# Performance work log

Hardware: AMD Instinct MI355X
Metric: run time of the kernel (lower is better)

The kernel has to match this reference:

```python
import jax, jax.numpy as jnp
import numpy as np

B, S, D, H = 2, 2048, 512, 8
DK = D // H  # 64


def setup_inputs() -> dict:
    key = jax.random.key(0)
    ks = jax.random.split(key, 16)
    def t(k):
        return jax.random.normal(k, (B, S, D), dtype=jnp.float32)
    inp = {
        'query_real': t(ks[0]), 'key_real': t(ks[1]), 'value_real': t(ks[2]),
        'query_phase': t(ks[3]), 'key_phase': t(ks[4]), 'value_phase': t(ks[5]),
        'mask': jax.random.randint(ks[6], (B, 1, S), 0, 2, dtype=jnp.int32),
    }
    # Four distinct linear layers (clones deepcopies); real and phase paths share them.
    for i, nm in enumerate(['q', 'k', 'v', 'o']):
        inp['W' + nm] = jax.random.normal(ks[7 + 2 * i], (D, D), dtype=jnp.float32) * 0.02
        inp['b' + nm] = jax.random.normal(ks[8 + 2 * i], (D,), dtype=jnp.float32) * 0.02
    return inp


def _lin(x, W, b):
    # nn.Linear: x @ W.T + b
    return jnp.einsum('bsd,ed->bse', x, W) + b


def _heads(x):
    # [B,S,D] -> [B,H,S,DK]
    return jnp.swapaxes(x.reshape(B, S, H, DK), 1, 2)


def reference(query_real, key_real, value_real, query_phase, key_phase, value_phase,
              mask, Wq, bq, Wk, bk, Wv, bv, Wo, bo):
    qr = _heads(_lin(query_real, Wq, bq)); qp = _heads(_lin(query_phase, Wq, bq))
    kr = _heads(_lin(key_real, Wk, bk));   kp = _heads(_lin(key_phase, Wk, bk))
    vr = _heads(_lin(value_real, Wv, bv)); vp = _heads(_lin(value_phase, Wv, bv))

    # complex QK^T: 4 matmuls -> real/imag parts, magnitude score
    sr = jnp.einsum('bhqd,bhkd->bhqk', qr, kr) - jnp.einsum('bhqd,bhkd->bhqk', qp, kp)
    sp = jnp.einsum('bhqd,bhkd->bhqk', qr, kp) + jnp.einsum('bhqd,bhkd->bhqk', qp, kr)
    scores = jnp.sqrt(sr * sr + sp * sp) / jnp.sqrt(jnp.float32(DK))
    # mask [B,1,S] -> unsqueeze head dim -> [B,1,1,S]
    scores = jnp.where(mask[:, None] == 0, jnp.float32(-1e9), scores)
    p = jax.nn.softmax(scores, axis=-1)

    xr = jnp.einsum('bhqk,bhkd->bhqd', p, vr)
    xp = jnp.einsum('bhqk,bhkd->bhqd', p, vp)
    xr = jnp.swapaxes(xr, 1, 2).reshape(B, S, D)
    xp = jnp.swapaxes(xp, 1, 2).reshape(B, S, D)
    return _lin(xr, Wo, bo), _lin(xp, Wo, bo)
```

## Files before the change

kernel.cpp:

```cpp
#include <hip/hip_runtime.h>

typedef __bf16 bf16;
typedef __bf16 bf16x8 __attribute__((ext_vector_type(8)));
typedef float  f32x4  __attribute__((ext_vector_type(4)));

static constexpr int CB = 2;
static constexpr int CS = 2048;
static constexpr int CD = 512;
static constexpr int CH = 8;
static constexpr int CDK = 64;
static constexpr int NROWS = CB * CH * CS;
static constexpr size_t NT = (size_t)CB * CS * CD;
static constexpr size_t WN = (size_t)CD * CD;

__device__ __forceinline__ f32x4 mfma16(bf16x8 a, bf16x8 b, f32x4 c) {
    return __builtin_amdgcn_mfma_f32_16x16x32_bf16(a, b, c, 0, 0, 0);
}

__device__ __forceinline__ bf16x8 cvt8(const float* __restrict__ p) {
    float4 x0 = *reinterpret_cast<const float4*>(p);
    float4 x1 = *reinterpret_cast<const float4*>(p + 4);
    bf16x8 r;
    r[0] = (bf16)x0.x; r[1] = (bf16)x0.y; r[2] = (bf16)x0.z; r[3] = (bf16)x0.w;
    r[4] = (bf16)x1.x; r[5] = (bf16)x1.y; r[6] = (bf16)x1.z; r[7] = (bf16)x1.w;
    return r;
}

__device__ __forceinline__ void gload16(const void* g, void* l) {
    __builtin_amdgcn_global_load_lds(
        (const __attribute__((address_space(1))) void*)g,
        (__attribute__((address_space(3))) void*)l, 16, 0, 0);
}

struct CvtP {
    const float* src[10];
    bf16* dst[10];
    int n8[10];
};
__global__ __launch_bounds__(256) void cvt_kernel(CvtP C) {
    const int t = blockIdx.y;
    const int i = blockIdx.x * 256 + threadIdx.x;
    if (i < C.n8[t])
        *reinterpret_cast<bf16x8*>(C.dst[t] + (size_t)i * 8) =
            cvt8(C.src[t] + (size_t)i * 8);
}

struct PB {
    const bf16* A[6];
    const bf16* W[6];
    const float* bias[6];
    bf16* dst[6];
    int mode[6];
};
__global__ __launch_bounds__(256) void projb_kernel(PB P) {
    __shared__ uint4 tile[2][2][512];

    const int z = blockIdx.z;
    const bf16* __restrict__ A = P.A[z];
    const bf16* __restrict__ W = P.W[z];
    const float* __restrict__ bias = P.bias[z];
    bf16* __restrict__ dst = P.dst[z];
    const int mode = P.mode[z];

    const int m0 = blockIdx.x * 64, n0 = blockIdx.y * 64;
    const int tid = threadIdx.x;
    const int lane = tid & 63, w = tid >> 6;
    const int wm = w >> 1, wn = w & 1;
    const int l16 = lane & 15, lhi = lane >> 4;

    const int tensor = w >> 1, half = w & 1;
    const int rlo = lane >> 3, slotL = lane & 7;
    const bf16* gbase = tensor ? W : A;
    const int t0 = tensor ? n0 : m0;
    const char* gp = (const char*)gbase
                   + (size_t)(t0 + half*32 + rlo) * (CD * 2)
                   + (size_t)((slotL ^ rlo) * 16);

    auto stage = [&](int buf, int kk) {
        const char* p = gp + (size_t)kk * 128;
        uint4* ld = &tile[buf][tensor][half * 256];
        #pragma unroll
        for (int i = 0; i < 4; ++i)
            gload16(p + (size_t)i * 8 * (CD * 2), ld + i * 64);
    };

    f32x4 acc[2][2] = {};

    stage(0, 0);
    asm volatile("s_waitcnt vmcnt(0)" ::: "memory");
    __syncthreads();

    for (int kk = 0; kk < 8; ++kk) {
        if (kk + 1 < 8) stage((kk + 1) & 1, kk + 1);

        const uint4* aT = &tile[kk & 1][0][0];
        const uint4* bT = &tile[kk & 1][1][0];
        #pragma unroll
        for (int ks = 0; ks < 2; ++ks) {
            const int c = ks*4 + lhi;
            const int ra0 = wm*32 + l16, ra1 = ra0 + 16;
            const int rb0 = wn*32 + l16, rb1 = rb0 + 16;
            bf16x8 af0 = __builtin_bit_cast(bf16x8, aT[ra0*8 + (c ^ (ra0 & 7))]);
            bf16x8 af1 = __builtin_bit_cast(bf16x8, aT[ra1*8 + (c ^ (ra1 & 7))]);
            bf16x8 bg0 = __builtin_bit_cast(bf16x8, bT[rb0*8 + (c ^ (rb0 & 7))]);
            bf16x8 bg1 = __builtin_bit_cast(bf16x8, bT[rb1*8 + (c ^ (rb1 & 7))]);
            acc[0][0] = mfma16(af0, bg0, acc[0][0]);
            acc[0][1] = mfma16(af0, bg1, acc[0][1]);
            acc[1][0] = mfma16(af1, bg0, acc[1][0]);
            acc[1][1] = mfma16(af1, bg1, acc[1][1]);
        }
        if (kk + 1 < 8) __syncthreads();
    }

    #pragma unroll
    for (int ms = 0; ms < 2; ++ms)
    #pragma unroll
    for (int ns = 0; ns < 2; ++ns) {
        const int col = n0 + wn*32 + ns*16 + l16;
        const float bv = bias[col];
        const int hh = col >> 6, dk = col & 63;
        #pragma unroll
        for (int i = 0; i < 4; ++i) {
            const int m = m0 + wm*32 + ms*16 + lhi*4 + i;
            const float v = acc[ms][ns][i] + bv;
            const int b = m >> 11, s = m & 2047;
            if (mode == 0)
                dst[(((size_t)(b*CH + hh)) * CS + s) * CDK + dk] = (bf16)v;
            else
                dst[(((size_t)(b*CH + hh)) * CDK + dk) * CS + s] = (bf16)v;
        }
    }
}

__global__ __launch_bounds__(256) void oprojb_kernel(
    const bf16* __restrict__ Xr, const bf16* __restrict__ Xp,
    const bf16* __restrict__ Wo, const float* __restrict__ bo,
    float* __restrict__ out)
{
    __shared__ uint4 tile[2][2][512];

    const bf16* __restrict__ A = blockIdx.z ? Xp : Xr;
    float* __restrict__ dst = out + (size_t)blockIdx.z * NT;

    const int m0 = blockIdx.x * 64, n0 = blockIdx.y * 64;
    const int tid = threadIdx.x;
    const int lane = tid & 63, w = tid >> 6;
    const int wm = w >> 1, wn = w & 1;
    const int l16 = lane & 15, lhi = lane >> 4;

    const int tensor = w >> 1, half = w & 1;
    const int rlo = lane >> 3, slotL = lane & 7;
    const bf16* gbase = tensor ? Wo : A;
    const int t0 = tensor ? n0 : m0;
    const char* gp = (const char*)gbase
                   + (size_t)(t0 + half*32 + rlo) * (CD * 2)
                   + (size_t)((slotL ^ rlo) * 16);

    auto stage = [&](int buf, int kk) {
        const char* p = gp + (size_t)kk * 128;
        uint4* ld = &tile[buf][tensor][half * 256];
        #pragma unroll
        for (int i = 0; i < 4; ++i)
            gload16(p + (size_t)i * 8 * (CD * 2), ld + i * 64);
    };

    f32x4 acc[2][2] = {};

    stage(0, 0);
    asm volatile("s_waitcnt vmcnt(0)" ::: "memory");
    __syncthreads();

    for (int kk = 0; kk < 8; ++kk) {
        if (kk + 1 < 8) stage((kk + 1) & 1, kk + 1);

        const uint4* aT = &tile[kk & 1][0][0];
        const uint4* bT = &tile[kk & 1][1][0];
        #pragma unroll
        for (int ks = 0; ks < 2; ++ks) {
            const int c = ks*4 + lhi;
            const int ra0 = wm*32 + l16, ra1 = ra0 + 16;
            const int rb0 = wn*32 + l16, rb1 = rb0 + 16;
            bf16x8 af0 = __builtin_bit_cast(bf16x8, aT[ra0*8 + (c ^ (ra0 & 7))]);
            bf16x8 af1 = __builtin_bit_cast(bf16x8, aT[ra1*8 + (c ^ (ra1 & 7))]);
            bf16x8 bg0 = __builtin_bit_cast(bf16x8, bT[rb0*8 + (c ^ (rb0 & 7))]);
            bf16x8 bg1 = __builtin_bit_cast(bf16x8, bT[rb1*8 + (c ^ (rb1 & 7))]);
            acc[0][0] = mfma16(af0, bg0, acc[0][0]);
            acc[0][1] = mfma16(af0, bg1, acc[0][1]);
            acc[1][0] = mfma16(af1, bg0, acc[1][0]);
            acc[1][1] = mfma16(af1, bg1, acc[1][1]);
        }
        if (kk + 1 < 8) __syncthreads();
    }

    #pragma unroll
    for (int ms = 0; ms < 2; ++ms)
    #pragma unroll
    for (int ns = 0; ns < 2; ++ns) {
        const int col = n0 + wn*32 + ns*16 + l16;
        const float bv = bo[col];
        #pragma unroll
        for (int i = 0; i < 4; ++i) {
            const int m = m0 + wm*32 + ms*16 + lhi*4 + i;
            dst[(size_t)m * 512 + col] = acc[ms][ns][i] + bv;
        }
    }
}

__global__ __launch_bounds__(512, 4) void attn_kernel(
    const bf16* __restrict__ Qr, const bf16* __restrict__ Qp,
    const bf16* __restrict__ Kr, const bf16* __restrict__ Kp,
    const bf16* __restrict__ Vtr, const bf16* __restrict__ Vtp,
    const int* __restrict__ mask, int lognsp,
    float* __restrict__ POR, float* __restrict__ POP, float* __restrict__ PLs)
{
    __shared__ uint4 stg[2][4][512];

    const int F = blockIdx.x;
    const int qt = (F >> 3) & 15;
    const int g  = (F & 7) | ((F >> 7) << 3);
    const int bh = g >> lognsp, z = g & ((1 << lognsp) - 1);
    const int Lkv = CS >> lognsp, kvbase = z * Lkv;
    const int nt = Lkv >> 6;
    const int b = bh >> 3;
    const size_t base = (size_t)bh * CS * CDK;

    const int tid = threadIdx.x, lane = tid & 63, w = tid >> 6;
    const int l16 = lane & 15, lhi = lane >> 4;
    const int q0 = qt * 128 + w * 16;

    const int tensor = w >> 1, half = w & 1;
    const int rlo = lane >> 3, slotL = lane & 7;
    const int chunkL = slotL ^ rlo;
    const char* gsrc = (tensor == 0) ? (const char*)Kr : (tensor == 1) ? (const char*)Kp
                     : (tensor == 2) ? (const char*)Vtr : (const char*)Vtp;
    size_t laneoff, iStride, tStride;
    if (tensor < 2) {
        laneoff = base*2 + (size_t)(kvbase + half*32 + rlo) * 128 + chunkL*16;
        iStride = 8 * 128;  tStride = 8192;
    } else {
        laneoff = base*2 + (size_t)(half*32 + rlo) * (CS*2) + (size_t)kvbase*2 + chunkL*16;
        iStride = 8 * CS * 2;  tStride = 128;
    }
    const char* gp = gsrc + laneoff;

    auto stage = [&](int bi, int t) {
        const char* p = gp + (size_t)t * tStride;
        uint4* ldst = &stg[bi][tensor][half * 256];
        #pragma unroll
        for (int i = 0; i < 4; ++i)
            gload16(p + i*iStride, ldst + i*64);
    };

    stage(0, 0);

    bf16x8 qrf[2], qpf[2], qnf[2];
    #pragma unroll
    for (int ks = 0; ks < 2; ++ks) {
        const size_t qoff = base + (size_t)(q0 + l16) * CDK + ks*32 + lhi*8;
        qrf[ks] = *reinterpret_cast<const bf16x8*>(&Qr[qoff]);
        qpf[ks] = *reinterpret_cast<const bf16x8*>(&Qp[qoff]);
        uint4 t = __builtin_bit_cast(uint4, qpf[ks]);
        t.x ^= 0x80008000u; t.y ^= 0x80008000u; t.z ^= 0x80008000u; t.w ^= 0x80008000u;
        qnf[ks] = __builtin_bit_cast(bf16x8, t);
    }

    unsigned long long keepA[8] = {};
    for (int t = 0; t < nt; ++t) {
        const unsigned long long m64 =
            __ballot(mask[b*CS + kvbase + t*64 + lane] != 0);
        const unsigned long long s = m64 >> (lhi * 4);
        const unsigned int k16 = (unsigned int)(s & 0xFull)
                               | ((unsigned int)((s >> 16) & 0xFull) << 4)
                               | ((unsigned int)((s >> 32) & 0xFull) << 8)
                               | ((unsigned int)((s >> 48) & 0xFull) << 12);
        keepA[t >> 2] |= (unsigned long long)k16 << ((t & 3) * 16);
    }

    f32x4 oR[4] = {}, oP[4] = {};
    float lpart = 0.f;

    asm volatile("s_waitcnt vmcnt(0)" ::: "memory");
    __syncthreads();

    for (int t = 0; t < nt; ++t) {
        if (t + 1 < nt) stage((t + 1) & 1, t + 1);

        const int bi = t & 1;
        const unsigned int k16 = (unsigned int)(keepA[t >> 2] >> ((t & 3) * 16)) & 0xFFFFu;
        const uint4* kTr = &stg[bi][0][0];
        const uint4* kTp = &stg[bi][1][0];
        const uint4* vTr = &stg[bi][2][0];
        const uint4* vTp = &stg[bi][3][0];

        float pp[4][4];
        #pragma unroll
        for (int kb = 0; kb < 4; ++kb) {
            const int krow = kb*16 + l16;
            f32x4 aR = {}, aP = {};
            __builtin_amdgcn_s_setprio(1);
            #pragma unroll
            for (int ks = 0; ks < 2; ++ks) {
                const int ci = krow*8 + ((ks*4 + lhi) ^ (krow & 7));
                const bf16x8 kr8 = __builtin_bit_cast(bf16x8, kTr[ci]);
                const bf16x8 kp8 = __builtin_bit_cast(bf16x8, kTp[ci]);
                aR = mfma16(kr8, qrf[ks], aR);
                aR = mfma16(kp8, qnf[ks], aR);
                aP = mfma16(kr8, qpf[ks], aP);
                aP = mfma16(kp8, qrf[ks], aP);
            }
            __builtin_amdgcn_s_setprio(0);
            #pragma unroll
            for (int i = 0; i < 4; ++i) {
                const float sr = aR[i], sp = aP[i];
                const float mag = __builtin_amdgcn_sqrtf(fmaf(sr, sr, sp*sp));
                float p = __builtin_amdgcn_exp2f(fmaf(mag, 0.18033688f, -5.77078016f));
                p = ((k16 >> (kb*4 + i)) & 1u) ? p : 0.0f;
                pp[kb][i] = p;
                lpart += p;
            }
        }

        #pragma unroll
        for (int c = 0; c < 2; ++c) {
            unsigned int r0, r1, r2, r3;
            asm("v_cvt_pk_bf16_f32 %0, %1, %2" : "=v"(r0) : "v"(pp[2*c][0]),   "v"(pp[2*c][1]));
            asm("v_cvt_pk_bf16_f32 %0, %1, %2" : "=v"(r1) : "v"(pp[2*c][2]),   "v"(pp[2*c][3]));
            asm("v_cvt_pk_bf16_f32 %0, %1, %2" : "=v"(r2) : "v"(pp[2*c+1][0]), "v"(pp[2*c+1][1]));
            asm("v_cvt_pk_bf16_f32 %0, %1, %2" : "=v"(r3) : "v"(pp[2*c+1][2]), "v"(pp[2*c+1][3]));
            asm volatile("v_permlane32_swap_b32 %0, %1" : "+v"(r0), "+v"(r2));
            asm volatile("v_permlane32_swap_b32 %0, %1" : "+v"(r1), "+v"(r3));
            asm volatile("v_permlane16_swap_b32 %0, %1" : "+v"(r0), "+v"(r2));
            asm volatile("v_permlane16_swap_b32 %0, %1" : "+v"(r1), "+v"(r3));
            uint4 fw; fw.x = r0; fw.y = r1; fw.z = r2; fw.w = r3;
            const bf16x8 pa = __builtin_bit_cast(bf16x8, fw);
            __builtin_amdgcn_s_setprio(1);
            #pragma unroll
            for (int dt = 0; dt < 4; ++dt) {
                const int vrow = dt*16 + l16;
                const int ci = vrow*8 + ((c*4 + lhi) ^ (vrow & 7));
                oR[dt] = mfma16(__builtin_bit_cast(bf16x8, vTr[ci]), pa, oR[dt]);
                oP[dt] = mfma16(__builtin_bit_cast(bf16x8, vTp[ci]), pa, oP[dt]);
            }
            __builtin_amdgcn_s_setprio(0);
        }

        if (t + 1 < nt) __syncthreads();
    }

    {
        float v = lpart;
        v += __shfl_xor(v, 16);
        v += __shfl_xor(v, 32);
        lpart = v;
    }
    const int r0q = bh * CS + q0;
    if (lane < 16)
        PLs[(size_t)z * NROWS + r0q + lane] = lpart;

    const size_t zo = (size_t)z * NROWS * 64;
    #pragma unroll
    for (int dt = 0; dt < 4; ++dt) {
        const size_t off = zo + (size_t)(r0q + l16) * 64 + dt*16 + lhi*4;
        *reinterpret_cast<f32x4*>(&POR[off]) = oR[dt];
        *reinterpret_cast<f32x4*>(&POP[off]) = oP[dt];
    }
}

__global__ __launch_bounds__(256) void merge_kernel(
    const float* __restrict__ POR, const float* __restrict__ POP,
    const float* __restrict__ PLs, int nsp,
    bf16* __restrict__ Xr, bf16* __restrict__ Xp)
{
    const int idx = blockIdx.x * 256 + threadIdx.x;
    const int r = idx >> 4, c0 = (idx & 15) * 4;
    float l = 0.f;
    f32x4 orv = {}, opv = {};
    for (int zz = 0; zz < nsp; ++zz) {
        l += PLs[(size_t)zz * NROWS + r];
        const size_t o = (size_t)zz * NROWS * 64 + (size_t)r * 64 + c0;
        orv += *reinterpret_cast<const f32x4*>(&POR[o]);
        opv += *reinterpret_cast<const f32x4*>(&POP[o]);
    }
    const float inv = 1.f / l;
    const int bh = r >> 11, q = r & 2047;
    const int b = bh >> 3, h = bh & 7;
    const size_t off = ((size_t)(b*CS + q)) * CD + h*CDK + c0;
    bf16 vr[4], vp[4];
    #pragma unroll
    for (int j = 0; j < 4; ++j) { vr[j] = (bf16)(orv[j]*inv); vp[j] = (bf16)(opv[j]*inv); }
    *reinterpret_cast<uint2*>(&Xr[off]) = *reinterpret_cast<const uint2*>(vr);
    *reinterpret_cast<uint2*>(&Xp[off]) = *reinterpret_cast<const uint2*>(vp);
}

extern "C" void kernel_launch(void* const* d_in, const int* in_sizes, int n_in,
                              void* d_out, int out_size, void* d_ws, size_t ws_size,
                              hipStream_t stream) {
    const float* q_r = (const float*)d_in[0];
    const float* k_r = (const float*)d_in[1];
    const float* v_r = (const float*)d_in[2];
    const float* q_p = (const float*)d_in[3];
    const float* k_p = (const float*)d_in[4];
    const float* v_p = (const float*)d_in[5];
    const int*  mask = (const int*)d_in[6];
    const float* Wq = (const float*)d_in[7];  const float* bq = (const float*)d_in[8];
    const float* Wk = (const float*)d_in[9];  const float* bk = (const float*)d_in[10];
    const float* Wv = (const float*)d_in[11]; const float* bv = (const float*)d_in[12];
    const float* Wo = (const float*)d_in[13]; const float* bo = (const float*)d_in[14];
    float* out = (float*)d_out;

    bf16* ws = (bf16*)d_ws;
    bf16* Abf = ws;
    bf16* Wbf = ws + 6 * NT;
    bf16* Qr  = Wbf + 4 * WN;
    bf16 *Qp = Qr + NT, *Kr = Qp + NT, *Kp = Kr + NT;
    bf16 *Vtr = Kp + NT, *Vtp = Vtr + NT;
    bf16 *Xr = Vtp + NT, *Xp = Xr + NT;
    float* POR = (float*)(Xp + NT);

    const size_t fixedB = (14 * NT + 4 * WN) * sizeof(bf16);
    const size_t per_split = (size_t)NROWS * 64 * 4 * 2 + (size_t)NROWS * 4;
    int nsp, lognsp;
    if (ws_size >= fixedB + 2 * per_split) { nsp = 2; lognsp = 1; }
    else                                   { nsp = 1; lognsp = 0; }
    float* POP = POR + (size_t)nsp * NROWS * 64;
    float* PLs = POP + (size_t)nsp * NROWS * 64;

    dim3 blk(256);

    CvtP C;
    C.src[0]=q_r; C.src[1]=q_p; C.src[2]=k_r; C.src[3]=k_p; C.src[4]=v_r; C.src[5]=v_p;
    C.src[6]=Wq;  C.src[7]=Wk;  C.src[8]=Wv;  C.src[9]=Wo;
    for (int i = 0; i < 6; ++i) { C.dst[i] = Abf + (size_t)i * NT; C.n8[i] = (int)(NT / 8); }
    for (int i = 0; i < 4; ++i) { C.dst[6+i] = Wbf + (size_t)i * WN; C.n8[6+i] = (int)(WN / 8); }
    cvt_kernel<<<dim3((unsigned)(NT / 8 / 256), 10), blk, 0, stream>>>(C);

    PB P;
    for (int i = 0; i < 6; ++i) P.A[i] = Abf + (size_t)i * NT;
    P.W[0]=Wbf;      P.W[1]=Wbf;      P.W[2]=Wbf+WN;   P.W[3]=Wbf+WN;
    P.W[4]=Wbf+2*WN; P.W[5]=Wbf+2*WN;
    P.bias[0]=bq; P.bias[1]=bq; P.bias[2]=bk; P.bias[3]=bk; P.bias[4]=bv; P.bias[5]=bv;
    P.dst[0]=Qr; P.dst[1]=Qp; P.dst[2]=Kr; P.dst[3]=Kp; P.dst[4]=Vtr; P.dst[5]=Vtp;
    P.mode[0]=0; P.mode[1]=0; P.mode[2]=0; P.mode[3]=0; P.mode[4]=1; P.mode[5]=1;
    projb_kernel<<<dim3(64, 8, 6), blk, 0, stream>>>(P);

    attn_kernel<<<dim3(256 * nsp), dim3(512), 0, stream>>>(Qr, Qp, Kr, Kp, Vtr, Vtp,
                                                           mask, lognsp, POR, POP, PLs);

    merge_kernel<<<dim3(NROWS * 16 / 256), blk, 0, stream>>>(POR, POP, PLs, nsp, Xr, Xp);

    oprojb_kernel<<<dim3(64, 8, 2), blk, 0, stream>>>(Xr, Xp, Wbf + 3 * WN, bo, out);
}
```

Before: 122.7 us.

## Load K fragments directly from global into registers, stage only V in LDS

K tiles are no longer staged through shared memory. Each wave reads its K fragments straight from global memory with a one-step register prefetch, while only Vt is double-buffered in LDS. This halves LDS usage, which may allow more resident blocks and fewer LDS reads. In exchange, every wave fetches K redundantly from global memory, and the sign flip for the imaginary term is now applied to K inside the inner loop rather than once to Q.

```diff
diff --git a/kernel.cpp b/kernel.cpp
--- a/kernel.cpp
+++ b/kernel.cpp
@@ -213,7 +213,7 @@
     const int* __restrict__ mask, int lognsp,
     float* __restrict__ POR, float* __restrict__ POP, float* __restrict__ PLs)
 {
-    __shared__ uint4 stg[2][4][512];
+    __shared__ uint4 vstg[2][2][512];
 
     const int F = blockIdx.x;
     const int qt = (F >> 3) & 15;
@@ -228,40 +228,29 @@
     const int l16 = lane & 15, lhi = lane >> 4;
     const int q0 = qt * 128 + w * 16;
 
-    const int tensor = w >> 1, half = w & 1;
+    const int vtensor = w & 1, quarter = w >> 1;
     const int rlo = lane >> 3, slotL = lane & 7;
     const int chunkL = slotL ^ rlo;
-    const char* gsrc = (tensor == 0) ? (const char*)Kr : (tensor == 1) ? (const char*)Kp
-                     : (tensor == 2) ? (const char*)Vtr : (const char*)Vtp;
-    size_t laneoff, iStride, tStride;
-    if (tensor < 2) {
-        laneoff = base*2 + (size_t)(kvbase + half*32 + rlo) * 128 + chunkL*16;
-        iStride = 8 * 128;  tStride = 8192;
-    } else {
-        laneoff = base*2 + (size_t)(half*32 + rlo) * (CS*2) + (size_t)kvbase*2 + chunkL*16;
-        iStride = 8 * CS * 2;  tStride = 128;
-    }
-    const char* gp = gsrc + laneoff;
-
-    auto stage = [&](int bi, int t) {
-        const char* p = gp + (size_t)t * tStride;
-        uint4* ldst = &stg[bi][tensor][half * 256];
-        #pragma unroll
-        for (int i = 0; i < 4; ++i)
-            gload16(p + i*iStride, ldst + i*64);
+    const char* vgsrc = vtensor ? (const char*)Vtp : (const char*)Vtr;
+    const char* vgp = vgsrc + base*2 + (size_t)(quarter*16 + rlo) * (CS*2)
+                    + (size_t)kvbase*2 + chunkL*16;
+
+    auto stageV = [&](int bi, int t) {
+        const char* p = vgp + (size_t)t * 128;
+        uint4* ld = &vstg[bi][vtensor][quarter * 128];
+        #pragma unroll
+        for (int i = 0; i < 2; ++i)
+            gload16(p + (size_t)i * (8 * CS * 2), ld + i * 64);
     };
 
-    stage(0, 0);
-
-    bf16x8 qrf[2], qpf[2], qnf[2];
+    stageV(0, 0);
+
+    bf16x8 qrf[2], qpf[2];
     #pragma unroll
     for (int ks = 0; ks < 2; ++ks) {
         const size_t qoff = base + (size_t)(q0 + l16) * CDK + ks*32 + lhi*8;
         qrf[ks] = *reinterpret_cast<const bf16x8*>(&Qr[qoff]);
         qpf[ks] = *reinterpret_cast<const bf16x8*>(&Qp[qoff]);
-        uint4 t = __builtin_bit_cast(uint4, qpf[ks]);
-        t.x ^= 0x80008000u; t.y ^= 0x80008000u; t.z ^= 0x80008000u; t.w ^= 0x80008000u;
-        qnf[ks] = __builtin_bit_cast(bf16x8, t);
     }
 
     unsigned long long keepA[8] = {};
@@ -283,28 +272,44 @@
     __syncthreads();
 
     for (int t = 0; t < nt; ++t) {
-        if (t + 1 < nt) stage((t + 1) & 1, t + 1);
-
-        const int bi = t & 1;
+        if (t + 1 < nt) stageV((t + 1) & 1, t + 1);
+
+        const int kvg = kvbase + t * 64;
         const unsigned int k16 = (unsigned int)(keepA[t >> 2] >> ((t & 3) * 16)) & 0xFFFFu;
-        const uint4* kTr = &stg[bi][0][0];
-        const uint4* kTp = &stg[bi][1][0];
-        const uint4* vTr = &stg[bi][2][0];
-        const uint4* vTp = &stg[bi][3][0];
+
+        const bf16* kbase_r = Kr + base + (size_t)kvg * CDK + lhi*8;
+        const bf16* kbase_p = Kp + base + (size_t)kvg * CDK + lhi*8;
+        bf16x8 krr[2][2], kpp[2][2];
+        #pragma unroll
+        for (int ks = 0; ks < 2; ++ks) {
+            krr[0][ks] = *reinterpret_cast<const bf16x8*>(kbase_r + (size_t)l16*CDK + ks*32);
+            kpp[0][ks] = *reinterpret_cast<const bf16x8*>(kbase_p + (size_t)l16*CDK + ks*32);
+        }
 
         float pp[4][4];
         #pragma unroll
         for (int kb = 0; kb < 4; ++kb) {
-            const int krow = kb*16 + l16;
+            if (kb < 3) {
+                const size_t ro = (size_t)((kb + 1)*16 + l16) * CDK;
+                #pragma unroll
+                for (int ks = 0; ks < 2; ++ks) {
+                    krr[(kb + 1) & 1][ks] = *reinterpret_cast<const bf16x8*>(kbase_r + ro + ks*32);
+                    kpp[(kb + 1) & 1][ks] = *reinterpret_cast<const bf16x8*>(kbase_p + ro + ks*32);
+                }
+            }
+            const int par = kb & 1;
             f32x4 aR = {}, aP = {};
             __builtin_amdgcn_s_setprio(1);
             #pragma unroll
             for (int ks = 0; ks < 2; ++ks) {
-                const int ci = krow*8 + ((ks*4 + lhi) ^ (krow & 7));
-                const bf16x8 kr8 = __builtin_bit_cast(bf16x8, kTr[ci]);
-                const bf16x8 kp8 = __builtin_bit_cast(bf16x8, kTp[ci]);
+                const bf16x8 kr8 = krr[par][ks];
+                const bf16x8 kp8 = kpp[par][ks];
+                uint4 tn = __builtin_bit_cast(uint4, kp8);
+                tn.x ^= 0x80008000u; tn.y ^= 0x80008000u;
+                tn.z ^= 0x80008000u; tn.w ^= 0x80008000u;
+                const bf16x8 kn8 = __builtin_bit_cast(bf16x8, tn);
                 aR = mfma16(kr8, qrf[ks], aR);
-                aR = mfma16(kp8, qnf[ks], aR);
+                aR = mfma16(kn8, qpf[ks], aR);
                 aP = mfma16(kr8, qpf[ks], aP);
                 aP = mfma16(kp8, qrf[ks], aP);
             }
@@ -338,8 +343,10 @@
             for (int dt = 0; dt < 4; ++dt) {
                 const int vrow = dt*16 + l16;
                 const int ci = vrow*8 + ((c*4 + lhi) ^ (vrow & 7));
-                oR[dt] = mfma16(__builtin_bit_cast(bf16x8, vTr[ci]), pa, oR[dt]);
-                oP[dt] = mfma16(__builtin_bit_cast(bf16x8, vTp[ci]), pa, oP[dt]);
+                const bf16x8 v8r = __builtin_bit_cast(bf16x8, vstg[t & 1][0][ci]);
+                const bf16x8 v8p = __builtin_bit_cast(bf16x8, vstg[t & 1][1][ci]);
+                oR[dt] = mfma16(v8r, pa, oR[dt]);
+                oP[dt] = mfma16(v8p, pa, oP[dt]);
             }
             __builtin_amdgcn_s_setprio(0);
         }
```

Result: slower. 197.7 us (+61.1%).
